# Kernel tuning notes

Measured on AMD Instinct MI355X. Metric: run time of the kernel, lower is better.

Reference implementation:

```python
import jax, jax.numpy as jnp
import numpy as np

B = 4096           # batch
F = 16             # categorical fields
V = 50000          # vocab per field
D = 128            # embed_dim
T = 2              # task_num
ES = 8             # specific_expert_num
ESH = 8            # shared_expert_num
NUMN = 63          # numerical_num
IN0 = (F + 1) * D  # 2176 = embed_output_dim
H0, H1 = 512, 256  # bottom_mlp_dims
INV = float(1.0 / np.sqrt(1.0 + 1e-5))  # eval BatchNorm1d: running_mean=0, running_var=1


def setup_inputs():
    keys = iter(jax.random.split(jax.random.key(0), 64))
    def nrm(shape, s=0.02):
        return jax.random.normal(next(keys), shape, jnp.float32) * s
    inp = {}
    inp["categorical_x"] = jax.random.randint(next(keys), (B, F), 0, V)
    inp["numerical_x"] = jax.random.normal(next(keys), (B, NUMN), jnp.float32)
    inp["emb_table"] = nrm((F * V, D))
    inp["num_W"] = nrm((NUMN, D)); inp["num_b"] = jnp.zeros((D,), jnp.float32)
    def mlp(prefix, lead, i, o):
        inp[prefix + "_W"] = nrm(lead + (i, o))
        inp[prefix + "_b"] = jnp.zeros(lead + (o,), jnp.float32)
        inp[prefix + "_g"] = jnp.ones(lead + (o,), jnp.float32)    # BN gamma
        inp[prefix + "_be"] = jnp.zeros(lead + (o,), jnp.float32)  # BN beta
    # PLE layer 0 (input dim IN0 -> H0)
    mlp("se0", (ESH,), IN0, H0); mlp("te0", (T, ES), IN0, H0)
    inp["tg0_W"] = nrm((T, IN0, ES + ESH)); inp["tg0_b"] = jnp.zeros((T, ES + ESH), jnp.float32)
    inp["sg0_W"] = nrm((IN0, T * ES + ESH)); inp["sg0_b"] = jnp.zeros((T * ES + ESH,), jnp.float32)
    # PLE layer 1 (H0 -> H1); share gate of last layer is unused in torch forward
    mlp("se1", (ESH,), H0, H1); mlp("te1", (T, ES), H0, H1)
    inp["tg1_W"] = nrm((T, H0, ES + ESH)); inp["tg1_b"] = jnp.zeros((T, ES + ESH), jnp.float32)
    # per-task towers: [H1->128]->BN->ReLU, [128->64]->BN->ReLU, [64->1]
    mlp("tw0", (T,), H1, 128); mlp("tw1", (T,), 128, 64)
    inp["two_W"] = nrm((T, 64, 1)); inp["two_b"] = jnp.zeros((T, 1), jnp.float32)
    return inp


def _ple_layer(shared, tfea, seW, seb, seg, sebe, teW, teb, teg, tebe, tgW, tgb, sgW=None, sgb=None):
    # shared: [B, in]; tfea: [T, B, in]
    nT, nB = tfea.shape[0], tfea.shape[1]
    # shared experts: [B, ESH, o]
    sh = jax.nn.relu((jnp.einsum('bi,eio->beo', shared, seW) + seb) * INV * seg + sebe)
    # task-specific experts: [T, B, ES, o]
    th = jnp.einsum('tbi,teio->tbeo', tfea, teW) + teb[:, None]
    th = jax.nn.relu(th * INV * teg[:, None] + tebe[:, None])
    # per-task gates over [own ES experts ++ shared ESH experts]
    gate = jax.nn.softmax(jnp.einsum('tbi,tig->tbg', tfea, tgW) + tgb[:, None], axis=-1)
    mix = jnp.concatenate([th, jnp.broadcast_to(sh[None], (nT,) + sh.shape)], axis=2)
    new_t = jnp.einsum('tbg,tbgo->tbo', gate, mix)
    if sgW is None:  # last layer: shared branch not updated
        return None, new_t
    # shared gate over [all tasks' experts (task order) ++ shared experts]
    all_mix = jnp.concatenate(
        [jnp.transpose(th, (1, 0, 2, 3)).reshape(nB, nT * th.shape[2], th.shape[3]), sh], axis=1)
    g2 = jax.nn.softmax(shared @ sgW + sgb, axis=-1)
    new_s = jnp.einsum('bg,bgo->bo', g2, all_mix)
    return new_s, new_t


def reference(categorical_x, numerical_x, emb_table, num_W, num_b,
              se0_W, se0_b, se0_g, se0_be, te0_W, te0_b, te0_g, te0_be, tg0_W, tg0_b, sg0_W, sg0_b,
              se1_W, se1_b, se1_g, se1_be, te1_W, te1_b, te1_g, te1_be, tg1_W, tg1_b,
              tw0_W, tw0_b, tw0_g, tw0_be, tw1_W, tw1_b, tw1_g, tw1_be, two_W, two_b):
    offsets = jnp.arange(F) * V
    cat_emb = emb_table[categorical_x + offsets]                         # [B,F,D]
    num_emb = numerical_x @ num_W + num_b                                # [B,D]
    emb = jnp.concatenate([cat_emb.reshape(B, F * D), num_emb], axis=1)  # [B,IN0]
    shared = emb
    tfea = jnp.broadcast_to(emb[None], (T, B, IN0))
    shared, tfea = _ple_layer(shared, tfea, se0_W, se0_b, se0_g, se0_be,
                              te0_W, te0_b, te0_g, te0_be, tg0_W, tg0_b, sg0_W, sg0_b)
    _, tfea = _ple_layer(shared, tfea, se1_W, se1_b, se1_g, se1_be,
                         te1_W, te1_b, te1_g, te1_be, tg1_W, tg1_b)
    # towers (eval BN, dropout identity)
    h = jax.nn.relu((jnp.einsum('tbi,tio->tbo', tfea, tw0_W) + tw0_b[:, None]) * INV * tw0_g[:, None] + tw0_be[:, None])
    h = jax.nn.relu((jnp.einsum('tbi,tio->tbo', h, tw1_W) + tw1_b[:, None]) * INV * tw1_g[:, None] + tw1_be[:, None])
    out = jnp.einsum('tbi,tio->tbo', h, two_W) + two_b[:, None]          # [T,B,1]
    return jax.nn.sigmoid(out[..., 0])                                   # [T,B]
```

## Files before the change

kernel.cpp:

```cpp
#include <hip/hip_runtime.h>

typedef unsigned short u16;
typedef unsigned int u32;
typedef __attribute__((ext_vector_type(4))) u16 u16x4;
typedef __attribute__((ext_vector_type(8))) __bf16 bf16x8;
typedef __attribute__((ext_vector_type(4))) float floatx4;

#define INV_BN 0.9999950000374997f
#define IN0 2176
#define N0EXT 12416
#define N1EXT 2176

__device__ __forceinline__ float b2f(u16 u) {
  return __builtin_bit_cast(float, (u32)u << 16);
}
__device__ __forceinline__ u16 f2b(float f) {
  u32 x = __builtin_bit_cast(u32, f);
  return (u16)((x + 0x7fffu + ((x >> 16) & 1u)) >> 16);
}

__global__ __launch_bounds__(256) void embed_gather(
    const int* __restrict__ cat, const float* __restrict__ table,
    u16* __restrict__ X0) {
  int idx = blockIdx.x * 256 + threadIdx.x;
  int d4 = idx & 31;
  int bf = idx >> 5;
  int f = bf & 15;
  int b = bf >> 4;
  long row = (long)cat[bf] + (long)f * 50000;
  float4 v = *((const float4*)(table + row * 128) + d4);
  u16x4 o = {f2b(v.x), f2b(v.y), f2b(v.z), f2b(v.w)};
  *(u16x4*)(X0 + (long)b * IN0 + f * 128 + d4 * 4) = o;
}

__global__ __launch_bounds__(256) void num_linear(
    const float* __restrict__ xn, const float* __restrict__ W,
    const float* __restrict__ bias, u16* __restrict__ X0) {
  int idx = blockIdx.x * 256 + threadIdx.x;
  int o = idx & 127;
  int b = idx >> 7;
  float acc = bias[o];
  const float* xr = xn + b * 63;
  for (int k = 0; k < 63; k++) acc = fmaf(xr[k], W[k * 128 + o], acc);
  X0[(long)b * IN0 + 2048 + o] = f2b(acc);
}

__global__ __launch_bounds__(256) void repack_w(
    const float* __restrict__ src, const float* __restrict__ gsc,
    u16* __restrict__ dst, int K, int O, int nBase) {
  __shared__ float tile[32][33];
  int e = blockIdx.z;
  int k0 = blockIdx.x * 32, o0 = blockIdx.y * 32;
  int tx = threadIdx.x & 31, ty = threadIdx.x >> 5;
  const float* S = src + (long)e * K * O;
#pragma unroll
  for (int r = 0; r < 32; r += 8)
    tile[ty + r][tx] = S[(long)(k0 + ty + r) * O + o0 + tx];
  __syncthreads();
#pragma unroll
  for (int r = 0; r < 32; r += 8) {
    int o = o0 + ty + r;
    float s = INV_BN * gsc[e * O + o];
    dst[(long)(nBase + e * O + o) * K + k0 + tx] = f2b(tile[tx][ty + r] * s);
  }
}

__global__ __launch_bounds__(256) void repack_gates0(
    const float* __restrict__ tgW, const float* __restrict__ tgb,
    const float* __restrict__ sgW, const float* __restrict__ sgb,
    u16* __restrict__ W0, float* __restrict__ bias0) {
  int g = blockIdx.x;
  u16* dst = W0 + (long)(12288 + g) * IN0;
  for (int k = threadIdx.x; k < IN0; k += 256) {
    float v;
    if (g < 32) {
      int t = g >> 4, j = g & 15;
      v = tgW[(long)t * IN0 * 16 + k * 16 + j];
    } else if (g < 56) {
      v = sgW[k * 24 + (g - 32)];
    } else {
      v = 0.f;
    }
    dst[k] = f2b(v);
  }
  if (threadIdx.x == 0)
    bias0[12288 + g] = g < 32 ? tgb[g] : (g < 56 ? sgb[g - 32] : 0.f);
}

__global__ __launch_bounds__(256) void repack_gates1(
    const float* __restrict__ tgW, const float* __restrict__ tgb,
    u16* __restrict__ W1, float* __restrict__ bias1) {
  int g = blockIdx.x;
  int z = blockIdx.y;
  u16* dst = W1 + (long)z * N1EXT * 512 + (long)(2048 + g) * 512;
  for (int k = threadIdx.x; k < 512; k += 256) {
    float v = (z < 2 && g < 16) ? tgW[(long)z * 512 * 16 + k * 16 + g] : 0.f;
    dst[k] = f2b(v);
  }
  if (threadIdx.x == 0)
    bias1[z * N1EXT + 2048 + g] = (z < 2 && g < 16) ? tgb[z * 16 + g] : 0.f;
}

__global__ __launch_bounds__(128) void repack_tw1(
    const float* __restrict__ W, const float* __restrict__ g,
    const float* __restrict__ b, const float* __restrict__ be,
    u16* __restrict__ TW1, float* __restrict__ biasT1) {
  int n = blockIdx.x;
  int z = blockIdx.y;
  int k = threadIdx.x;
  float v = 0.f;
  if (n < 64) v = W[(long)z * 128 * 64 + k * 64 + n] * INV_BN * g[z * 64 + n];
  TW1[(long)z * 128 * 128 + n * 128 + k] = f2b(v);
  if (k == 0)
    biasT1[z * 128 + n] =
        (n < 64) ? b[z * 64 + n] * INV_BN * g[z * 64 + n] + be[z * 64 + n] : 0.f;
}

__global__ __launch_bounds__(256) void fuse_bias(
    const float* __restrict__ b, const float* __restrict__ g,
    const float* __restrict__ be, float* __restrict__ out, int n) {
  int i = blockIdx.x * 256 + threadIdx.x;
  if (i < n) out[i] = b[i] * INV_BN * g[i] + be[i];
}

__global__ __launch_bounds__(256) void gemm_bf16(
    const u16* __restrict__ A, long aStride,
    const u16* __restrict__ Bw, long bStride,
    u16* __restrict__ C, long cStride,
    const float* __restrict__ bias, long biasStride,
    int M, int N, int K, int reluN) {
  int z = blockIdx.z;
  A += (long)z * aStride;
  Bw += (long)z * bStride;
  C += (long)z * cStride;
  bias += (long)z * biasStride;
  __shared__ u16 As[128 * 32];
  __shared__ u16 Bs[128 * 32];
  int tid = threadIdx.x;
  int m0 = blockIdx.x * 128, n0 = blockIdx.y * 128;
  int l = tid & 63, w = tid >> 6;
  int wm = (w >> 1) * 64, wn = (w & 1) * 64;

  int qa = ((tid & 3) - (tid >> 3)) & 3;
  const u16* aS0 = A + (long)(m0 + (tid >> 2)) * K + qa * 8;
  const u16* aS1 = A + (long)(m0 + 64 + (tid >> 2)) * K + qa * 8;
  const u16* bS0 = Bw + (long)(n0 + (tid >> 2)) * K + qa * 8;
  const u16* bS1 = Bw + (long)(n0 + 64 + (tid >> 2)) * K + qa * 8;
  u16* aD0 = As + tid * 8;
  u16* aD1 = As + (256 + tid) * 8;
  u16* bD0 = Bs + tid * 8;
  u16* bD1 = Bs + (256 + tid) * 8;

  floatx4 acc[4][4] = {};

  int aOff[4], bOff[4];
  int q = l >> 4;
#pragma unroll
  for (int i = 0; i < 4; i++) {
    int Ra = wm + i * 16 + (l & 15);
    int Rb = wn + i * 16 + (l & 15);
    aOff[i] = Ra * 32 + ((q + (Ra >> 1)) & 3) * 8;
    bOff[i] = Rb * 32 + ((q + (Rb >> 1)) & 3) * 8;
  }

  for (int k0 = 0; k0 < K; k0 += 32) {
    __builtin_amdgcn_global_load_lds((const __attribute__((address_space(1))) u16*)aS0,
                                     (__attribute__((address_space(3))) u16*)aD0, 16, 0, 0);
    __builtin_amdgcn_global_load_lds((const __attribute__((address_space(1))) u16*)aS1,
                                     (__attribute__((address_space(3))) u16*)aD1, 16, 0, 0);
    __builtin_amdgcn_global_load_lds((const __attribute__((address_space(1))) u16*)bS0,
                                     (__attribute__((address_space(3))) u16*)bD0, 16, 0, 0);
    __builtin_amdgcn_global_load_lds((const __attribute__((address_space(1))) u16*)bS1,
                                     (__attribute__((address_space(3))) u16*)bD1, 16, 0, 0);
    aS0 += 32; aS1 += 32; bS0 += 32; bS1 += 32;
    __syncthreads();
    bf16x8 af[4], bfr[4];
#pragma unroll
    for (int i = 0; i < 4; i++) af[i] = *(const bf16x8*)(As + aOff[i]);
#pragma unroll
    for (int j = 0; j < 4; j++) bfr[j] = *(const bf16x8*)(Bs + bOff[j]);
#pragma unroll
    for (int i = 0; i < 4; i++)
#pragma unroll
      for (int j = 0; j < 4; j++)
        acc[i][j] = __builtin_amdgcn_mfma_f32_16x16x32_bf16(af[i], bfr[j], acc[i][j], 0, 0, 0);
    __syncthreads();
  }

  int cn = n0 + wn + (l & 15);
  int rm = m0 + wm + ((l >> 4) << 2);
#pragma unroll
  for (int j = 0; j < 4; j++) {
    int col = cn + j * 16;
    float bv = bias[col];
    bool doRelu = col < reluN;
#pragma unroll
    for (int i = 0; i < 4; i++)
#pragma unroll
      for (int r = 0; r < 4; r++) {
        float v = acc[i][j][r] + bv;
        v = doRelu ? fmaxf(v, 0.f) : v;
        C[(long)(rm + i * 16 + r) * N + col] = f2b(v);
      }
  }
}

__global__ __launch_bounds__(256) void mix0_kernel(
    const u16* __restrict__ E0, u16* __restrict__ X1) {
  int b = blockIdx.x, tid = threadIdx.x;
  __shared__ float gw[56];
  const u16* row = E0 + (long)b * N0EXT;
  if (tid < 3) {
    int base = (tid == 0) ? 0 : (tid == 1) ? 16 : 32;
    int cnt = (tid == 2) ? 24 : 16;
    const u16* lg = row + 12288 + base;
    float mx = -1e30f;
    for (int i = 0; i < cnt; i++) mx = fmaxf(mx, b2f(lg[i]));
    float sum = 0.f;
    for (int i = 0; i < cnt; i++) {
      float e = __expf(b2f(lg[i]) - mx);
      gw[base + i] = e;
      sum += e;
    }
    float inv = 1.f / sum;
    for (int i = 0; i < cnt; i++) gw[base + i] *= inv;
  }
  __syncthreads();
#pragma unroll
  for (int half = 0; half < 2; half++) {
    int o = tid + half * 256;
    float t0 = 0.f, t1 = 0.f, s = 0.f;
#pragma unroll
    for (int e = 0; e < 8; e++) {
      float v0 = b2f(row[e * 512 + o]);
      float v1 = b2f(row[(8 + e) * 512 + o]);
      float vs = b2f(row[(16 + e) * 512 + o]);
      t0 = fmaf(gw[e], v0, t0);       t0 = fmaf(gw[8 + e], vs, t0);
      t1 = fmaf(gw[16 + e], v1, t1);  t1 = fmaf(gw[24 + e], vs, t1);
      s = fmaf(gw[32 + e], v0, s);
      s = fmaf(gw[40 + e], v1, s);
      s = fmaf(gw[48 + e], vs, s);
    }
    X1[((long)(0 * 4096 + b)) * 512 + o] = f2b(t0);
    X1[((long)(1 * 4096 + b)) * 512 + o] = f2b(t1);
    X1[((long)(2 * 4096 + b)) * 512 + o] = f2b(s);
  }
}

__global__ __launch_bounds__(256) void mix1_kernel(
    const u16* __restrict__ E1, u16* __restrict__ X2) {
  int b = blockIdx.x, tid = threadIdx.x;
  __shared__ float gw[32];
  if (tid < 2) {
    const u16* lg = E1 + ((long)(tid * 4096 + b)) * N1EXT + 2048;
    float mx = -1e30f;
    for (int i = 0; i < 16; i++) mx = fmaxf(mx, b2f(lg[i]));
    float sum = 0.f;
    for (int i = 0; i < 16; i++) {
      float e = __expf(b2f(lg[i]) - mx);
      gw[tid * 16 + i] = e;
      sum += e;
    }
    float inv = 1.f / sum;
    for (int i = 0; i < 16; i++) gw[tid * 16 + i] *= inv;
  }
  __syncthreads();
  int o = tid;
  const u16* r0 = E1 + ((long)(0 * 4096 + b)) * N1EXT;
  const u16* r1 = E1 + ((long)(1 * 4096 + b)) * N1EXT;
  const u16* rs = E1 + ((long)(2 * 4096 + b)) * N1EXT;
  float t0 = 0.f, t1 = 0.f;
#pragma unroll
  for (int e = 0; e < 8; e++) {
    float vs = b2f(rs[e * 256 + o]);
    t0 = fmaf(gw[e], b2f(r0[e * 256 + o]), t0);
    t0 = fmaf(gw[8 + e], vs, t0);
    t1 = fmaf(gw[16 + e], b2f(r1[e * 256 + o]), t1);
    t1 = fmaf(gw[24 + e], vs, t1);
  }
  X2[((long)(0 * 4096 + b)) * 256 + o] = f2b(t0);
  X2[((long)(1 * 4096 + b)) * 256 + o] = f2b(t1);
}

__global__ __launch_bounds__(256) void final_kernel(
    const u16* __restrict__ H2, const float* __restrict__ twoW,
    const float* __restrict__ twob, float* __restrict__ out) {
  int idx = blockIdx.x * 256 + threadIdx.x;
  int t = idx >> 12, b = idx & 4095;
  const u16* xr = H2 + ((long)(t * 4096 + b)) * 128;
  const float* wc = twoW + t * 64;
  float acc = twob[t];
  for (int k = 0; k < 64; k++) acc = fmaf(b2f(xr[k]), wc[k], acc);
  out[t * 4096 + b] = 1.f / (1.f + __expf(-acc));
}

extern "C" void kernel_launch(void* const* d_in, const int* in_sizes, int n_in,
                              void* d_out, int out_size, void* d_ws, size_t ws_size,
                              hipStream_t stream) {
  const int* cat = (const int*)d_in[0];
  const float* numx = (const float*)d_in[1];
  const float* table = (const float*)d_in[2];
  const float* numW = (const float*)d_in[3];
  const float* numb = (const float*)d_in[4];
  const float* se0W = (const float*)d_in[5];
  const float* se0b = (const float*)d_in[6];
  const float* se0g = (const float*)d_in[7];
  const float* se0be = (const float*)d_in[8];
  const float* te0W = (const float*)d_in[9];
  const float* te0b = (const float*)d_in[10];
  const float* te0g = (const float*)d_in[11];
  const float* te0be = (const float*)d_in[12];
  const float* tg0W = (const float*)d_in[13];
  const float* tg0b = (const float*)d_in[14];
  const float* sg0W = (const float*)d_in[15];
  const float* sg0b = (const float*)d_in[16];
  const float* se1W = (const float*)d_in[17];
  const float* se1b = (const float*)d_in[18];
  const float* se1g = (const float*)d_in[19];
  const float* se1be = (const float*)d_in[20];
  const float* te1W = (const float*)d_in[21];
  const float* te1b = (const float*)d_in[22];
  const float* te1g = (const float*)d_in[23];
  const float* te1be = (const float*)d_in[24];
  const float* tg1W = (const float*)d_in[25];
  const float* tg1b = (const float*)d_in[26];
  const float* tw0W = (const float*)d_in[27];
  const float* tw0b = (const float*)d_in[28];
  const float* tw0g = (const float*)d_in[29];
  const float* tw0be = (const float*)d_in[30];
  const float* tw1W = (const float*)d_in[31];
  const float* tw1b = (const float*)d_in[32];
  const float* tw1g = (const float*)d_in[33];
  const float* tw1be = (const float*)d_in[34];
  const float* twoW = (const float*)d_in[35];
  const float* twob = (const float*)d_in[36];
  float* out = (float*)d_out;

  char* p = (char*)d_ws;
  u16* X0 = (u16*)p;        p += (size_t)4096 * IN0 * 2;
  u16* W0 = (u16*)p;        p += (size_t)N0EXT * IN0 * 2;
  float* bias0 = (float*)p; p += (size_t)N0EXT * 4;
  u16* X1 = (u16*)p;        p += (size_t)3 * 4096 * 512 * 2;
  u16* W1 = (u16*)p;        p += (size_t)3 * N1EXT * 512 * 2;
  float* bias1 = (float*)p; p += (size_t)3 * N1EXT * 4;
  u16* X2 = (u16*)p;        p += (size_t)2 * 4096 * 256 * 2;
  u16* TW0 = (u16*)p;       p += (size_t)2 * 128 * 256 * 2;
  float* biasT0 = (float*)p; p += (size_t)256 * 4;
  u16* TW1 = (u16*)p;       p += (size_t)2 * 128 * 128 * 2;
  float* biasT1 = (float*)p; p += (size_t)256 * 4;
  u16* E0 = (u16*)p;
  u16* E1 = (u16*)p;
  u16* H1 = (u16*)p;
  u16* H2 = H1 + (size_t)2 * 4096 * 128;

  embed_gather<<<8192, 256, 0, stream>>>(cat, table, X0);
  num_linear<<<2048, 256, 0, stream>>>(numx, numW, numb, X0);

  repack_w<<<dim3(68, 16, 16), 256, 0, stream>>>(te0W, te0g, W0, IN0, 512, 0);
  repack_w<<<dim3(68, 16, 8), 256, 0, stream>>>(se0W, se0g, W0, IN0, 512, 8192);
  repack_gates0<<<128, 256, 0, stream>>>(tg0W, tg0b, sg0W, sg0b, W0, bias0);
  repack_w<<<dim3(16, 8, 8), 256, 0, stream>>>(te1W, te1g, W1, 512, 256, 0);
  repack_w<<<dim3(16, 8, 8), 256, 0, stream>>>(te1W + (size_t)8 * 512 * 256, te1g + 8 * 256,
                                               W1, 512, 256, N1EXT);
  repack_w<<<dim3(16, 8, 8), 256, 0, stream>>>(se1W, se1g, W1, 512, 256, 2 * N1EXT);
  repack_gates1<<<dim3(128, 3), 256, 0, stream>>>(tg1W, tg1b, W1, bias1);
  fuse_bias<<<32, 256, 0, stream>>>(te0b, te0g, te0be, bias0, 8192);
  fuse_bias<<<16, 256, 0, stream>>>(se0b, se0g, se0be, bias0 + 8192, 4096);
  fuse_bias<<<8, 256, 0, stream>>>(te1b, te1g, te1be, bias1, 2048);
  fuse_bias<<<8, 256, 0, stream>>>(te1b + 2048, te1g + 2048, te1be + 2048, bias1 + N1EXT, 2048);
  fuse_bias<<<8, 256, 0, stream>>>(se1b, se1g, se1be, bias1 + 2 * N1EXT, 2048);
  repack_w<<<dim3(8, 4, 2), 256, 0, stream>>>(tw0W, tw0g, TW0, 256, 128, 0);
  fuse_bias<<<1, 256, 0, stream>>>(tw0b, tw0g, tw0be, biasT0, 256);
  repack_tw1<<<dim3(128, 2), 128, 0, stream>>>(tw1W, tw1g, tw1b, tw1be, TW1, biasT1);

  gemm_bf16<<<dim3(32, 97, 1), 256, 0, stream>>>(X0, 0, W0, 0, E0, 0, bias0, 0,
                                                 4096, N0EXT, IN0, 12288);
  mix0_kernel<<<4096, 256, 0, stream>>>(E0, X1);

  gemm_bf16<<<dim3(32, 17, 3), 256, 0, stream>>>(
      X1, (long)4096 * 512, W1, (long)N1EXT * 512, E1, (long)4096 * N1EXT,
      bias1, N1EXT, 4096, N1EXT, 512, 2048);
  mix1_kernel<<<4096, 256, 0, stream>>>(E1, X2);

  gemm_bf16<<<dim3(32, 1, 2), 256, 0, stream>>>(
      X2, (long)4096 * 256, TW0, (long)128 * 256, H1, (long)4096 * 128,
      biasT0, 128, 4096, 128, 256, 128);
  gemm_bf16<<<dim3(32, 1, 2), 256, 0, stream>>>(
      H1, (long)4096 * 128, TW1, (long)128 * 128, H2, (long)4096 * 128,
      biasT1, 128, 4096, 128, 128, 128);
  final_kernel<<<32, 256, 0, stream>>>(H2, twoW, twob, out);
}
```

Baseline: 1.054 ms.

## Merge setup kernels, fuse tower MLPs, split layer-0 GEMM, drop LDS swizzle

Merges the embedding gather and numeric linear into one launch, all weight repacks into one grid, and the small gate, bias and tower repacks into another. The two tower GEMMs and the final dot-plus-sigmoid become a single kernel that keeps intermediates in LDS. The layer-0 GEMM is split into two launches, and GEMM variants get compile-time N/K. The intent is to cut launch overhead and intermediate global traffic. The XOR-style LDS swizzle in the GEMM is removed, which may add LDS bank conflicts, and the merged repack grid launches many blocks that exit immediately.

```diff
diff --git a/kernel.cpp b/kernel.cpp
--- a/kernel.cpp
+++ b/kernel.cpp
@@ -19,37 +19,57 @@
   return (u16)((x + 0x7fffu + ((x >> 16) & 1u)) >> 16);
 }
 
-__global__ __launch_bounds__(256) void embed_gather(
+__global__ __launch_bounds__(256) void input_build(
     const int* __restrict__ cat, const float* __restrict__ table,
-    u16* __restrict__ X0) {
-  int idx = blockIdx.x * 256 + threadIdx.x;
-  int d4 = idx & 31;
-  int bf = idx >> 5;
-  int f = bf & 15;
-  int b = bf >> 4;
-  long row = (long)cat[bf] + (long)f * 50000;
-  float4 v = *((const float4*)(table + row * 128) + d4);
-  u16x4 o = {f2b(v.x), f2b(v.y), f2b(v.z), f2b(v.w)};
-  *(u16x4*)(X0 + (long)b * IN0 + f * 128 + d4 * 4) = o;
-}
-
-__global__ __launch_bounds__(256) void num_linear(
     const float* __restrict__ xn, const float* __restrict__ W,
     const float* __restrict__ bias, u16* __restrict__ X0) {
-  int idx = blockIdx.x * 256 + threadIdx.x;
-  int o = idx & 127;
-  int b = idx >> 7;
-  float acc = bias[o];
-  const float* xr = xn + b * 63;
-  for (int k = 0; k < 63; k++) acc = fmaf(xr[k], W[k * 128 + o], acc);
-  X0[(long)b * IN0 + 2048 + o] = f2b(acc);
-}
-
-__global__ __launch_bounds__(256) void repack_w(
-    const float* __restrict__ src, const float* __restrict__ gsc,
-    u16* __restrict__ dst, int K, int O, int nBase) {
+  int x = blockIdx.x, tid = threadIdx.x;
+  if (x < 8192) {
+    int idx = x * 256 + tid;
+    int d4 = idx & 31;
+    int bf = idx >> 5;
+    int f = bf & 15;
+    int b = bf >> 4;
+    long row = (long)cat[bf] + (long)f * 50000;
+    float4 v = *((const float4*)(table + row * 128) + d4);
+    u16x4 o = {f2b(v.x), f2b(v.y), f2b(v.z), f2b(v.w)};
+    *(u16x4*)(X0 + (long)b * IN0 + f * 128 + d4 * 4) = o;
+  } else {
+    int idx = (x - 8192) * 256 + tid;
+    int o = idx & 127;
+    int b = idx >> 7;
+    float acc = bias[o];
+    const float* xr = xn + b * 63;
+    for (int k = 0; k < 63; k++) acc = fmaf(xr[k], W[k * 128 + o], acc);
+    X0[(long)b * IN0 + 2048 + o] = f2b(acc);
+  }
+}
+
+__global__ __launch_bounds__(256) void repack_w_all(
+    const float* __restrict__ te0W, const float* __restrict__ te0g,
+    const float* __restrict__ se0W, const float* __restrict__ se0g,
+    const float* __restrict__ te1W, const float* __restrict__ te1g,
+    const float* __restrict__ se1W, const float* __restrict__ se1g,
+    const float* __restrict__ tw0W, const float* __restrict__ tw0g,
+    u16* __restrict__ W0, u16* __restrict__ W1, u16* __restrict__ TW0) {
+  int z = blockIdx.z;
+  const float *src, *gsc;
+  u16* dst;
+  int K, O, nBase, e, xm, ym;
+  if (z < 16) {
+    e = z; src = te0W; gsc = te0g; dst = W0; K = 2176; O = 512; nBase = 0; xm = 68; ym = 16;
+  } else if (z < 24) {
+    e = z - 16; src = se0W; gsc = se0g; dst = W0; K = 2176; O = 512; nBase = 8192; xm = 68; ym = 16;
+  } else if (z < 40) {
+    e = z - 24; src = te1W; gsc = te1g; dst = W1; K = 512; O = 256;
+    nBase = (e < 8) ? 0 : (N1EXT - 2048); xm = 16; ym = 8;
+  } else if (z < 48) {
+    e = z - 40; src = se1W; gsc = se1g; dst = W1; K = 512; O = 256; nBase = 2 * N1EXT; xm = 16; ym = 8;
+  } else {
+    e = z - 48; src = tw0W; gsc = tw0g; dst = TW0; K = 256; O = 128; nBase = 0; xm = 8; ym = 4;
+  }
+  if (blockIdx.x >= (u32)xm || blockIdx.y >= (u32)ym) return;
   __shared__ float tile[32][33];
-  int e = blockIdx.z;
   int k0 = blockIdx.x * 32, o0 = blockIdx.y * 32;
   int tx = threadIdx.x & 31, ty = threadIdx.x >> 5;
   const float* S = src + (long)e * K * O;
@@ -65,87 +85,90 @@
   }
 }
 
-__global__ __launch_bounds__(256) void repack_gates0(
-    const float* __restrict__ tgW, const float* __restrict__ tgb,
-    const float* __restrict__ sgW, const float* __restrict__ sgb,
-    u16* __restrict__ W0, float* __restrict__ bias0) {
-  int g = blockIdx.x;
-  u16* dst = W0 + (long)(12288 + g) * IN0;
-  for (int k = threadIdx.x; k < IN0; k += 256) {
+__global__ __launch_bounds__(256) void setup_small(
+    const float* __restrict__ tg0W, const float* __restrict__ tg0b,
+    const float* __restrict__ sg0W, const float* __restrict__ sg0b,
+    const float* __restrict__ tg1W, const float* __restrict__ tg1b,
+    const float* __restrict__ te0b, const float* __restrict__ te0g, const float* __restrict__ te0be,
+    const float* __restrict__ se0b, const float* __restrict__ se0g, const float* __restrict__ se0be,
+    const float* __restrict__ te1b, const float* __restrict__ te1g, const float* __restrict__ te1be,
+    const float* __restrict__ se1b, const float* __restrict__ se1g, const float* __restrict__ se1be,
+    const float* __restrict__ tw0b, const float* __restrict__ tw0g, const float* __restrict__ tw0be,
+    const float* __restrict__ tw1W, const float* __restrict__ tw1b,
+    const float* __restrict__ tw1g, const float* __restrict__ tw1be,
+    u16* __restrict__ W0, u16* __restrict__ W1, u16* __restrict__ TW1,
+    float* __restrict__ bias0, float* __restrict__ bias1,
+    float* __restrict__ biasT0, float* __restrict__ biasT1) {
+  int x = blockIdx.x, tid = threadIdx.x;
+  if (x < 128) {
+    int g = x;
+    u16* dst = W0 + (long)(12288 + g) * IN0;
+    for (int k = tid; k < IN0; k += 256) {
+      float v;
+      if (g < 32) {
+        int t = g >> 4, j = g & 15;
+        v = tg0W[(long)t * IN0 * 16 + k * 16 + j];
+      } else if (g < 56) {
+        v = sg0W[k * 24 + (g - 32)];
+      } else {
+        v = 0.f;
+      }
+      dst[k] = f2b(v);
+    }
+    if (tid == 0)
+      bias0[12288 + g] = g < 32 ? tg0b[g] : (g < 56 ? sg0b[g - 32] : 0.f);
+  } else if (x < 512) {
+    int i = x - 128;
+    int z = i >> 7, g = i & 127;
+    u16* dst = W1 + (long)z * N1EXT * 512 + (long)(2048 + g) * 512;
+    for (int k = tid; k < 512; k += 256) {
+      float v = (z < 2 && g < 16) ? tg1W[(long)z * 512 * 16 + k * 16 + g] : 0.f;
+      dst[k] = f2b(v);
+    }
+    if (tid == 0)
+      bias1[z * N1EXT + 2048 + g] = (z < 2 && g < 16) ? tg1b[z * 16 + g] : 0.f;
+  } else if (x < 640) {
+    int idx = (x - 512) * 256 + tid;
+    int z = idx >> 14, rem = idx & 16383, n = rem >> 7, k = rem & 127;
+    float v = 0.f;
+    if (n < 64) v = tw1W[(long)z * 128 * 64 + k * 64 + n] * INV_BN * tw1g[z * 64 + n];
+    TW1[(long)z * 128 * 128 + n * 128 + k] = f2b(v);
+    if (k == 0)
+      biasT1[z * 128 + n] =
+          (n < 64) ? tw1b[z * 64 + n] * INV_BN * tw1g[z * 64 + n] + tw1be[z * 64 + n] : 0.f;
+  } else if (x < 688) {
+    int i = (x - 640) * 256 + tid;
+    if (i < 8192) bias0[i] = te0b[i] * INV_BN * te0g[i] + te0be[i];
+    else {
+      int r = i - 8192;
+      bias0[i] = se0b[r] * INV_BN * se0g[r] + se0be[r];
+    }
+  } else if (x < 712) {
+    int j = (x - 688) * 256 + tid;
+    int z = j >> 11, r = j & 2047;
     float v;
-    if (g < 32) {
-      int t = g >> 4, j = g & 15;
-      v = tgW[(long)t * IN0 * 16 + k * 16 + j];
-    } else if (g < 56) {
-      v = sgW[k * 24 + (g - 32)];
-    } else {
-      v = 0.f;
-    }
-    dst[k] = f2b(v);
-  }
-  if (threadIdx.x == 0)
-    bias0[12288 + g] = g < 32 ? tgb[g] : (g < 56 ? sgb[g - 32] : 0.f);
-}
-
-__global__ __launch_bounds__(256) void repack_gates1(
-    const float* __restrict__ tgW, const float* __restrict__ tgb,
-    u16* __restrict__ W1, float* __restrict__ bias1) {
-  int g = blockIdx.x;
-  int z = blockIdx.y;
-  u16* dst = W1 + (long)z * N1EXT * 512 + (long)(2048 + g) * 512;
-  for (int k = threadIdx.x; k < 512; k += 256) {
-    float v = (z < 2 && g < 16) ? tgW[(long)z * 512 * 16 + k * 16 + g] : 0.f;
-    dst[k] = f2b(v);
-  }
-  if (threadIdx.x == 0)
-    bias1[z * N1EXT + 2048 + g] = (z < 2 && g < 16) ? tgb[z * 16 + g] : 0.f;
-}
-
-__global__ __launch_bounds__(128) void repack_tw1(
-    const float* __restrict__ W, const float* __restrict__ g,
-    const float* __restrict__ b, const float* __restrict__ be,
-    u16* __restrict__ TW1, float* __restrict__ biasT1) {
-  int n = blockIdx.x;
-  int z = blockIdx.y;
-  int k = threadIdx.x;
-  float v = 0.f;
-  if (n < 64) v = W[(long)z * 128 * 64 + k * 64 + n] * INV_BN * g[z * 64 + n];
-  TW1[(long)z * 128 * 128 + n * 128 + k] = f2b(v);
-  if (k == 0)
-    biasT1[z * 128 + n] =
-        (n < 64) ? b[z * 64 + n] * INV_BN * g[z * 64 + n] + be[z * 64 + n] : 0.f;
-}
-
-__global__ __launch_bounds__(256) void fuse_bias(
-    const float* __restrict__ b, const float* __restrict__ g,
-    const float* __restrict__ be, float* __restrict__ out, int n) {
-  int i = blockIdx.x * 256 + threadIdx.x;
-  if (i < n) out[i] = b[i] * INV_BN * g[i] + be[i];
-}
-
-__global__ __launch_bounds__(256) void gemm_bf16(
-    const u16* __restrict__ A, long aStride,
-    const u16* __restrict__ Bw, long bStride,
-    u16* __restrict__ C, long cStride,
-    const float* __restrict__ bias, long biasStride,
-    int M, int N, int K, int reluN) {
-  int z = blockIdx.z;
-  A += (long)z * aStride;
-  Bw += (long)z * bStride;
-  C += (long)z * cStride;
-  bias += (long)z * biasStride;
+    if (z < 2) v = te1b[z * 2048 + r] * INV_BN * te1g[z * 2048 + r] + te1be[z * 2048 + r];
+    else v = se1b[r] * INV_BN * se1g[r] + se1be[r];
+    bias1[z * N1EXT + r] = v;
+  } else {
+    biasT0[tid] = tw0b[tid] * INV_BN * tw0g[tid] + tw0be[tid];
+  }
+}
+
+__device__ __forceinline__ void gemm_body(
+    const u16* __restrict__ A, const u16* __restrict__ Bw, u16* __restrict__ C,
+    const float* __restrict__ bias, int N, int K, int reluN, int yOff) {
   __shared__ u16 As[128 * 32];
   __shared__ u16 Bs[128 * 32];
   int tid = threadIdx.x;
-  int m0 = blockIdx.x * 128, n0 = blockIdx.y * 128;
+  int m0 = blockIdx.x * 128, n0 = (blockIdx.y + yOff) * 128;
   int l = tid & 63, w = tid >> 6;
   int wm = (w >> 1) * 64, wn = (w & 1) * 64;
 
-  int qa = ((tid & 3) - (tid >> 3)) & 3;
-  const u16* aS0 = A + (long)(m0 + (tid >> 2)) * K + qa * 8;
-  const u16* aS1 = A + (long)(m0 + 64 + (tid >> 2)) * K + qa * 8;
-  const u16* bS0 = Bw + (long)(n0 + (tid >> 2)) * K + qa * 8;
-  const u16* bS1 = Bw + (long)(n0 + 64 + (tid >> 2)) * K + qa * 8;
+  const u16* aS0 = A + (long)(m0 + (tid >> 2)) * K + (tid & 3) * 8;
+  const u16* aS1 = A + (long)(m0 + 64 + (tid >> 2)) * K + (tid & 3) * 8;
+  const u16* bS0 = Bw + (long)(n0 + (tid >> 2)) * K + (tid & 3) * 8;
+  const u16* bS1 = Bw + (long)(n0 + 64 + (tid >> 2)) * K + (tid & 3) * 8;
   u16* aD0 = As + tid * 8;
   u16* aD1 = As + (256 + tid) * 8;
   u16* bD0 = Bs + tid * 8;
@@ -154,13 +177,10 @@
   floatx4 acc[4][4] = {};
 
   int aOff[4], bOff[4];
-  int q = l >> 4;
 #pragma unroll
   for (int i = 0; i < 4; i++) {
-    int Ra = wm + i * 16 + (l & 15);
-    int Rb = wn + i * 16 + (l & 15);
-    aOff[i] = Ra * 32 + ((q + (Ra >> 1)) & 3) * 8;
-    bOff[i] = Rb * 32 + ((q + (Rb >> 1)) & 3) * 8;
+    aOff[i] = (wm + i * 16 + (l & 15)) * 32 + (l >> 4) * 8;
+    bOff[i] = (wn + i * 16 + (l & 15)) * 32 + (l >> 4) * 8;
   }
 
   for (int k0 = 0; k0 < K; k0 += 32) {
@@ -203,6 +223,20 @@
         C[(long)(rm + i * 16 + r) * N + col] = f2b(v);
       }
   }
+}
+
+__global__ __launch_bounds__(256) void gemm_l0(
+    const u16* __restrict__ A, const u16* __restrict__ Bw, u16* __restrict__ C,
+    const float* __restrict__ bias, int yOff) {
+  gemm_body(A, Bw, C, bias, N0EXT, IN0, 12288, yOff);
+}
+
+__global__ __launch_bounds__(256) void gemm_l1(
+    const u16* __restrict__ A, const u16* __restrict__ Bw, u16* __restrict__ C,
+    const float* __restrict__ bias) {
+  int z = blockIdx.z;
+  gemm_body(A + (long)z * 4096 * 512, Bw + (long)z * N1EXT * 512,
+            C + (long)z * 4096 * N1EXT, bias + (long)z * N1EXT, N1EXT, 512, 2048, 0);
 }
 
 __global__ __launch_bounds__(256) void mix0_kernel(
@@ -282,16 +316,126 @@
   X2[((long)(1 * 4096 + b)) * 256 + o] = f2b(t1);
 }
 
-__global__ __launch_bounds__(256) void final_kernel(
-    const u16* __restrict__ H2, const float* __restrict__ twoW,
+__global__ __launch_bounds__(256) void towers_fused(
+    const u16* __restrict__ X2, const u16* __restrict__ TW0,
+    const u16* __restrict__ TW1, const float* __restrict__ biasT0,
+    const float* __restrict__ biasT1, const float* __restrict__ twoW,
     const float* __restrict__ twob, float* __restrict__ out) {
-  int idx = blockIdx.x * 256 + threadIdx.x;
-  int t = idx >> 12, b = idx & 4095;
-  const u16* xr = H2 + ((long)(t * 4096 + b)) * 128;
-  const float* wc = twoW + t * 64;
-  float acc = twob[t];
-  for (int k = 0; k < 64; k++) acc = fmaf(b2f(xr[k]), wc[k], acc);
-  out[t * 4096 + b] = 1.f / (1.f + __expf(-acc));
+  __shared__ u16 As[128 * 32];
+  __shared__ u16 Bs[128 * 32];
+  __shared__ u16 Hs[128 * 136];
+  int z = blockIdx.z;
+  int tid = threadIdx.x;
+  int m0 = blockIdx.x * 128;
+  int l = tid & 63, w = tid >> 6;
+  int wm = (w >> 1) * 64, wn = (w & 1) * 64;
+  int q = l >> 4;
+
+  const u16* A = X2 + (long)z * 4096 * 256;
+  const u16* B0 = TW0 + (long)z * 128 * 256;
+  const u16* B1 = TW1 + (long)z * 128 * 128;
+
+  int aOff[4], bOff[4];
+#pragma unroll
+  for (int i = 0; i < 4; i++) {
+    aOff[i] = (wm + i * 16 + (l & 15)) * 32 + q * 8;
+    bOff[i] = (wn + i * 16 + (l & 15)) * 32 + q * 8;
+  }
+  int rmLoc = wm + (q << 2);
+  int cnLoc = wn + (l & 15);
+
+  {
+    const u16* aS0 = A + (long)(m0 + (tid >> 2)) * 256 + (tid & 3) * 8;
+    const u16* aS1 = A + (long)(m0 + 64 + (tid >> 2)) * 256 + (tid & 3) * 8;
+    const u16* bS0 = B0 + (long)(tid >> 2) * 256 + (tid & 3) * 8;
+    const u16* bS1 = B0 + (long)(64 + (tid >> 2)) * 256 + (tid & 3) * 8;
+    u16* aD0 = As + tid * 8;
+    u16* aD1 = As + (256 + tid) * 8;
+    u16* bD0 = Bs + tid * 8;
+    u16* bD1 = Bs + (256 + tid) * 8;
+    floatx4 acc[4][4] = {};
+    for (int k0 = 0; k0 < 256; k0 += 32) {
+      __builtin_amdgcn_global_load_lds((const __attribute__((address_space(1))) u16*)aS0,
+                                       (__attribute__((address_space(3))) u16*)aD0, 16, 0, 0);
+      __builtin_amdgcn_global_load_lds((const __attribute__((address_space(1))) u16*)aS1,
+                                       (__attribute__((address_space(3))) u16*)aD1, 16, 0, 0);
+      __builtin_amdgcn_global_load_lds((const __attribute__((address_space(1))) u16*)bS0,
+                                       (__attribute__((address_space(3))) u16*)bD0, 16, 0, 0);
+      __builtin_amdgcn_global_load_lds((const __attribute__((address_space(1))) u16*)bS1,
+                                       (__attribute__((address_space(3))) u16*)bD1, 16, 0, 0);
+      aS0 += 32; aS1 += 32; bS0 += 32; bS1 += 32;
+      __syncthreads();
+      bf16x8 af[4], bfr[4];
+#pragma unroll
+      for (int i = 0; i < 4; i++) af[i] = *(const bf16x8*)(As + aOff[i]);
+#pragma unroll
+      for (int j = 0; j < 4; j++) bfr[j] = *(const bf16x8*)(Bs + bOff[j]);
+#pragma unroll
+      for (int i = 0; i < 4; i++)
+#pragma unroll
+        for (int j = 0; j < 4; j++)
+          acc[i][j] = __builtin_amdgcn_mfma_f32_16x16x32_bf16(af[i], bfr[j], acc[i][j], 0, 0, 0);
+      __syncthreads();
+    }
+#pragma unroll
+    for (int j = 0; j < 4; j++) {
+      int col = cnLoc + j * 16;
+      float bv = biasT0[z * 128 + col];
+#pragma unroll
+      for (int i = 0; i < 4; i++)
+#pragma unroll
+        for (int r = 0; r < 4; r++)
+          Hs[(rmLoc + i * 16 + r) * 136 + col] = f2b(fmaxf(acc[i][j][r] + bv, 0.f));
+    }
+  }
+  __syncthreads();
+
+  floatx4 acc2[4][4] = {};
+  {
+    const u16* bS0 = B1 + (long)(tid >> 2) * 128 + (tid & 3) * 8;
+    const u16* bS1 = B1 + (long)(64 + (tid >> 2)) * 128 + (tid & 3) * 8;
+    u16* bD0 = Bs + tid * 8;
+    u16* bD1 = Bs + (256 + tid) * 8;
+    for (int k0 = 0; k0 < 128; k0 += 32) {
+      __builtin_amdgcn_global_load_lds((const __attribute__((address_space(1))) u16*)bS0,
+                                       (__attribute__((address_space(3))) u16*)bD0, 16, 0, 0);
+      __builtin_amdgcn_global_load_lds((const __attribute__((address_space(1))) u16*)bS1,
+                                       (__attribute__((address_space(3))) u16*)bD1, 16, 0, 0);
+      bS0 += 32; bS1 += 32;
+      __syncthreads();
+      bf16x8 af[4], bfr[4];
+#pragma unroll
+      for (int i = 0; i < 4; i++)
+        af[i] = *(const bf16x8*)(Hs + (wm + i * 16 + (l & 15)) * 136 + k0 + q * 8);
+#pragma unroll
+      for (int j = 0; j < 4; j++) bfr[j] = *(const bf16x8*)(Bs + bOff[j]);
+#pragma unroll
+      for (int i = 0; i < 4; i++)
+#pragma unroll
+        for (int j = 0; j < 4; j++)
+          acc2[i][j] = __builtin_amdgcn_mfma_f32_16x16x32_bf16(af[i], bfr[j], acc2[i][j], 0, 0, 0);
+      __syncthreads();
+    }
+  }
+#pragma unroll
+  for (int j = 0; j < 4; j++) {
+    int col = cnLoc + j * 16;
+    float bv = biasT1[z * 128 + col];
+#pragma unroll
+    for (int i = 0; i < 4; i++)
+#pragma unroll
+      for (int r = 0; r < 4; r++)
+        Hs[(rmLoc + i * 16 + r) * 136 + col] = f2b(fmaxf(acc2[i][j][r] + bv, 0.f));
+  }
+  __syncthreads();
+
+  if (tid < 128) {
+    const float* wc = twoW + z * 64;
+    const u16* xr = Hs + tid * 136;
+    float acc = twob[z];
+    for (int k = 0; k < 64; k++) acc = fmaf(b2f(xr[k]), wc[k], acc);
+    out[z * 4096 + m0 + tid] = 1.f / (1.f + __expf(-acc));
+  }
 }
 
 extern "C" void kernel_launch(void* const* d_in, const int* in_sizes, int n_in,
@@ -350,43 +494,24 @@
   float* biasT1 = (float*)p; p += (size_t)256 * 4;
   u16* E0 = (u16*)p;
   u16* E1 = (u16*)p;
-  u16* H1 = (u16*)p;
-  u16* H2 = H1 + (size_t)2 * 4096 * 128;
-
-  embed_gather<<<8192, 256, 0, stream>>>(cat, table, X0);
-  num_linear<<<2048, 256, 0, stream>>>(numx, numW, numb, X0);
-
-  repack_w<<<dim3(68, 16, 16), 256, 0, stream>>>(te0W, te0g, W0, IN0, 512, 0);
-  repack_w<<<dim3(68, 16, 8), 256, 0, stream>>>(se0W, se0g, W0, IN0, 512, 8192);
-  repack_gates0<<<128, 256, 0, stream>>>(tg0W, tg0b, sg0W, sg0b, W0, bias0);
-  repack_w<<<dim3(16, 8, 8), 256, 0, stream>>>(te1W, te1g, W1, 512, 256, 0);
-  repack_w<<<dim3(16, 8, 8), 256, 0, stream>>>(te1W + (size_t)8 * 512 * 256, te1g + 8 * 256,
-                                               W1, 512, 256, N1EXT);
-  repack_w<<<dim3(16, 8, 8), 256, 0, stream>>>(se1W, se1g, W1, 512, 256, 2 * N1EXT);
-  repack_gates1<<<dim3(128, 3), 256, 0, stream>>>(tg1W, tg1b, W1, bias1);
-  fuse_bias<<<32, 256, 0, stream>>>(te0b, te0g, te0be, bias0, 8192);
-  fuse_bias<<<16, 256, 0, stream>>>(se0b, se0g, se0be, bias0 + 8192, 4096);
-  fuse_bias<<<8, 256, 0, stream>>>(te1b, te1g, te1be, bias1, 2048);
-  fuse_bias<<<8, 256, 0, stream>>>(te1b + 2048, te1g + 2048, te1be + 2048, bias1 + N1EXT, 2048);
-  fuse_bias<<<8, 256, 0, stream>>>(se1b, se1g, se1be, bias1 + 2 * N1EXT, 2048);
-  repack_w<<<dim3(8, 4, 2), 256, 0, stream>>>(tw0W, tw0g, TW0, 256, 128, 0);
-  fuse_bias<<<1, 256, 0, stream>>>(tw0b, tw0g, tw0be, biasT0, 256);
-  repack_tw1<<<dim3(128, 2), 128, 0, stream>>>(tw1W, tw1g, tw1b, tw1be, TW1, biasT1);
-
-  gemm_bf16<<<dim3(32, 97, 1), 256, 0, stream>>>(X0, 0, W0, 0, E0, 0, bias0, 0,
-                                                 4096, N0EXT, IN0, 12288);
+
+  input_build<<<10240, 256, 0, stream>>>(cat, table, numx, numW, numb, X0);
+  repack_w_all<<<dim3(68, 16, 50), 256, 0, stream>>>(
+      te0W, te0g, se0W, se0g, te1W, te1g, se1W, se1g, tw0W, tw0g, W0, W1, TW0);
+  setup_small<<<713, 256, 0, stream>>>(
+      tg0W, tg0b, sg0W, sg0b, tg1W, tg1b,
+      te0b, te0g, te0be, se0b, se0g, se0be,
+      te1b, te1g, te1be, se1b, se1g, se1be,
+      tw0b, tw0g, tw0be, tw1W, tw1b, tw1g, tw1be,
+      W0, W1, TW1, bias0, bias1, biasT0, biasT1);
+
+  gemm_l0<<<dim3(32, 49), 256, 0, stream>>>(X0, W0, E0, bias0, 0);
+  gemm_l0<<<dim3(32, 48), 256, 0, stream>>>(X0, W0, E0, bias0, 49);
   mix0_kernel<<<4096, 256, 0, stream>>>(E0, X1);
 
-  gemm_bf16<<<dim3(32, 17, 3), 256, 0, stream>>>(
-      X1, (long)4096 * 512, W1, (long)N1EXT * 512, E1, (long)4096 * N1EXT,
-      bias1, N1EXT, 4096, N1EXT, 512, 2048);
+  gemm_l1<<<dim3(32, 17, 3), 256, 0, stream>>>(X1, W1, E1, bias1);
   mix1_kernel<<<4096, 256, 0, stream>>>(E1, X2);
 
-  gemm_bf16<<<dim3(32, 1, 2), 256, 0, stream>>>(
-      X2, (long)4096 * 256, TW0, (long)128 * 256, H1, (long)4096 * 128,
-      biasT0, 128, 4096, 128, 256, 128);
-  gemm_bf16<<<dim3(32, 1, 2), 256, 0, stream>>>(
-      H1, (long)4096 * 128, TW1, (long)128 * 128, H2, (long)4096 * 128,
-      biasT1, 128, 4096, 128, 128, 128);
-  final_kernel<<<32, 256, 0, stream>>>(H2, twoW, twob, out);
-}
+  towers_fused<<<dim3(32, 1, 2), 256, 0, stream>>>(
+      X2, TW0, TW1, biasT0, biasT1, twoW, twob, out);
+}
```

New measurement: 972.1 us. 1.08x faster.
